# Optimization experiments

Hardware: AMD Instinct MI355X
Metric: run time of the kernel (lower is better)

The kernel has to match this reference:

```python
import jax, jax.numpy as jnp
import numpy as np

_SAMPLING_EPS = 1e-05
_FP16_TINY = float(np.finfo(np.float16).tiny)  # masked_fill value used by the torch code


def _token_mask(tokens, num_seqs, vocab_size):
    # bin-count via scatter-add into width vocab+1 (padding id == vocab), then mask
    rows = jnp.arange(num_seqs)[:, None]
    counts = jnp.zeros((num_seqs, vocab_size + 1), jnp.int32).at[rows, tokens].add(1)
    return counts[:, :vocab_size] > 0


def setup_inputs() -> dict:
    key = jax.random.key(0)
    ks = jax.random.split(key, 9)
    B, V, PL, OL = 128, 128000, 2048, 256
    logits = jax.random.normal(ks[0], (B, V), dtype=jnp.float32) * 4.0
    prompt_tokens = jax.random.randint(ks[1], (B, PL), 0, V, dtype=jnp.int64)
    output_tokens = jax.random.randint(ks[2], (B, OL), 0, V, dtype=jnp.int64)
    presence_penalties = jax.random.uniform(ks[3], (B,), dtype=jnp.float32)
    frequency_penalties = jax.random.uniform(ks[4], (B,), dtype=jnp.float32)
    repetition_penalties = 1.0 + 0.3 * jax.random.uniform(ks[5], (B,), dtype=jnp.float32)
    temperature = 0.1 + 0.9 * jax.random.uniform(ks[6], (B,), dtype=jnp.float32)
    top_k = jax.random.randint(ks[7], (B,), 1, 100, dtype=jnp.int64)
    top_p = 0.5 + 0.49 * jax.random.uniform(ks[8], (B,), dtype=jnp.float32)
    return {
        "logits": logits,
        "prompt_tokens": prompt_tokens,
        "output_tokens": output_tokens,
        "presence_penalties": presence_penalties,
        "frequency_penalties": frequency_penalties,
        "repetition_penalties": repetition_penalties,
        "temperature": temperature,
        "top_k": top_k,
        "top_p": top_p,
    }


def reference(logits, prompt_tokens, output_tokens, presence_penalties,
              frequency_penalties, repetition_penalties, temperature,
              top_k, top_p):
    B, V = logits.shape
    logits = logits.astype(jnp.float32)

    # --- penalties (NOTE: torch code computes frequency counts but never applies
    # frequency_penalties; we faithfully do the same) ---
    prompt_mask = _token_mask(prompt_tokens, B, V)
    output_mask = _token_mask(output_tokens, B, V)
    pen = jnp.where(prompt_mask | output_mask, repetition_penalties[:, None], 1.0)
    logits = jnp.where(logits > 0, logits / pen, logits * pen)
    logits = logits - presence_penalties[:, None] * output_mask.astype(jnp.float32)

    # --- temperature ---
    temp = jnp.where(temperature < _SAMPLING_EPS, 1.0, temperature)
    logits = logits / temp[:, None]

    # --- top-k / top-p via ascending sort (mirrors torch implementation) ---
    idx = jnp.argsort(logits, axis=-1)                      # ascending
    ls = jnp.take_along_axis(logits, idx, axis=-1)
    thr_pos = (V - top_k.astype(jnp.int32))[:, None]
    thr = jnp.take_along_axis(ls, thr_pos, axis=-1)         # [B,1]
    ls = jnp.where(ls < thr, _FP16_TINY, ls)
    probs_sort = jax.nn.softmax(ls, axis=-1)
    csum = jnp.cumsum(probs_sort, axis=-1)
    tp_mask = csum <= (1.0 - top_p)[:, None]
    tp_mask = tp_mask.at[:, -1].set(False)
    ls = jnp.where(tp_mask, _FP16_TINY, ls)

    # unsort back to original vocab order
    rows = jnp.arange(B)[:, None]
    out_logits = jnp.zeros_like(logits).at[rows, idx].set(ls)

    probs = jax.nn.softmax(out_logits, axis=-1)
    return probs, prompt_mask, output_mask
```

## Files before the change

kernel.cpp:

```cpp
#include <hip/hip_runtime.h>
#include <math.h>

#define B   128
#define V   128000
#define WPR 4000
#define PL  2048
#define OL  256
#define BPR 25
#define ITERS 5
#define TLOC 128
#define CAP  6144
#define FP16_TINY 6.103515625e-05f

#define HBINS 4096
#define HIDX(b) ((b) + ((b) >> 4))
#define HSZ (HBINS + (HBINS >> 4))

__device__ __forceinline__ unsigned key_of(float f) {
    unsigned u = __float_as_uint(f);
    unsigned m = (unsigned)(((int)u) >> 31) | 0x80000000u;
    return u ^ m;
}
__device__ __forceinline__ float key_inv(unsigned k) {
    unsigned u = (k & 0x80000000u) ? (k ^ 0x80000000u) : ~k;
    return __uint_as_float(u);
}

__device__ __forceinline__ float xform(float x, int pm, int om,
                                       float rp, float rrp, float pres, float itt) {
#pragma clang fp contract(off)
    float m = (pm | om) ? ((x > 0.0f) ? rrp : rp) : 1.0f;
    float l = x * m;
    if (om) l = l - pres;
    return l * itt;
}

__device__ __forceinline__ unsigned wave_suffix_u(unsigned x, int lane) {
#pragma unroll
    for (int o = 1; o < 64; o <<= 1) {
        unsigned a = __shfl_down(x, o);
        if (lane + o < 64) x += a;
    }
    return x;
}
__device__ __forceinline__ unsigned wave_prefix_u(unsigned x, int lane) {
#pragma unroll
    for (int o = 1; o < 64; o <<= 1) {
        unsigned a = __shfl_up(x, o);
        if (lane >= o) x += a;
    }
    return x;
}
__device__ __forceinline__ double wave_suffix_d(double x, int lane) {
#pragma unroll
    for (int o = 1; o < 64; o <<= 1) {
        double a = __shfl_down(x, o);
        if (lane + o < 64) x += a;
    }
    return x;
}
__device__ __forceinline__ double wave_sum_d(double x) {
#pragma unroll
    for (int o = 1; o < 64; o <<= 1) x += __shfl_xor(x, o);
    return x;
}
__device__ __forceinline__ unsigned wave_sum_u(unsigned x) {
#pragma unroll
    for (int o = 1; o < 64; o <<= 1) x += __shfl_xor(x, o);
    return x;
}

__global__ __launch_bounds__(256) void k_scatter(const int* __restrict__ ptok,
                                                 const int* __restrict__ otok,
                                                 unsigned* __restrict__ bitP,
                                                 unsigned* __restrict__ bitO,
                                                 unsigned* __restrict__ cnt) {
    __shared__ unsigned mp[WPR];
    __shared__ unsigned mo[WPR];
    int r = blockIdx.x;
    int t = threadIdx.x;
    for (int i = t; i < WPR; i += 256) { mp[i] = 0u; mo[i] = 0u; }
    if (t == 0) cnt[r] = 0u;
    __syncthreads();
    const int* prow = ptok + (size_t)r * PL;
    const int* orow = otok + (size_t)r * OL;
    for (int i = t; i < PL; i += 256) {
        int tok = prow[i];
        if ((unsigned)tok < (unsigned)V) atomicOr(&mp[tok >> 5], 1u << (tok & 31));
    }
    for (int i = t; i < OL; i += 256) {
        int tok = orow[i];
        if ((unsigned)tok < (unsigned)V) atomicOr(&mo[tok >> 5], 1u << (tok & 31));
    }
    __syncthreads();
    unsigned* bpo = bitP + (size_t)r * WPR;
    unsigned* boo = bitO + (size_t)r * WPR;
    for (int i = t; i < WPR; i += 256) { bpo[i] = mp[i]; boo[i] = mo[i]; }
}

__global__ __launch_bounds__(256) void k_main(
    const float* __restrict__ logits,
    const unsigned* __restrict__ bitP, const unsigned* __restrict__ bitO,
    const float* __restrict__ rep, const float* __restrict__ pres,
    const float* __restrict__ temp,
    float* __restrict__ outPm, float* __restrict__ outOm,
    unsigned* __restrict__ cnt, unsigned long long* __restrict__ cand)
{
    __shared__ unsigned h[HSZ];
    __shared__ unsigned wsum[4];
    __shared__ int s_beta;
    __shared__ unsigned s_base;
    int r = blockIdx.y;
    int c0 = blockIdx.x * (ITERS * 1024);
    int t = threadIdx.x;
    int lane = t & 63, wid = t >> 6;
    for (int i = t; i < HSZ; i += 256) h[i] = 0u;
    __syncthreads();
    float rp = rep[r], pp = pres[r];
    float tt = temp[r]; tt = (tt < 1e-5f) ? 1.0f : tt;
    float rrp = 1.0f / rp;
    float itt = 1.0f / tt;
    const float* lrow = logits + (size_t)r * V;
    float* pmrow = outPm + (size_t)r * V;
    float* omrow = outOm + (size_t)r * V;
    const unsigned* bp = bitP + (size_t)r * WPR;
    const unsigned* bo = bitO + (size_t)r * WPR;
    uint4 kv4[ITERS];
#pragma unroll
    for (int it = 0; it < ITERS; it++) {
        int i = c0 + it * 1024 + t * 4;
        float4 x = *(const float4*)(lrow + i);
        unsigned wp = bp[i >> 5], wo = bo[i >> 5];
        int sh = i & 31;
        float xs[4] = {x.x, x.y, x.z, x.w};
        unsigned ks[4];
        float fp[4], fo[4];
#pragma unroll
        for (int j = 0; j < 4; j++) {
            int p = (wp >> (sh + j)) & 1;
            int o = (wo >> (sh + j)) & 1;
            float l = xform(xs[j], p, o, rp, rrp, pp, itt);
            unsigned key = key_of(l);
            atomicAdd(&h[HIDX(key >> 20)], 1u);
            ks[j] = key; fp[j] = (float)p; fo[j] = (float)o;
        }
        kv4[it] = make_uint4(ks[0], ks[1], ks[2], ks[3]);
        *(float4*)(pmrow + i) = make_float4(fp[0], fp[1], fp[2], fp[3]);
        *(float4*)(omrow + i) = make_float4(fo[0], fo[1], fo[2], fo[3]);
    }
    __syncthreads();
    unsigned cs = 0;
#pragma unroll
    for (int j = 0; j < 16; j++) cs += h[HIDX(t * 16 + j)];
    unsigned sfx = wave_suffix_u(cs, lane);
    if (lane == 0) wsum[wid] = sfx;
    __syncthreads();
    unsigned suf = sfx;
#pragma unroll
    for (int w2 = 0; w2 < 4; w2++) if (w2 > wid) suf += wsum[w2];
    unsigned Snext = suf - cs;
    if (suf >= TLOC && Snext < TLOC) {
        unsigned run = Snext;
        int beta = t * 16;
        for (int j = 15; j >= 0; j--) {
            run += h[HIDX(t * 16 + j)];
            if (run >= TLOC) { beta = t * 16 + j; break; }
        }
        s_beta = beta;
    }
    __syncthreads();
    unsigned beta = (unsigned)s_beta;
    unsigned myc = 0;
#pragma unroll
    for (int it = 0; it < ITERS; it++) {
        unsigned ks[4] = {kv4[it].x, kv4[it].y, kv4[it].z, kv4[it].w};
#pragma unroll
        for (int j = 0; j < 4; j++)
            if ((ks[j] >> 20) >= beta) myc++;
    }
    unsigned pfx = wave_prefix_u(myc, lane);
    if (lane == 63) wsum[wid] = pfx;
    __syncthreads();
    unsigned pv = pfx;
#pragma unroll
    for (int w2 = 0; w2 < 4; w2++) if (w2 < wid) pv += wsum[w2];
    if (t == 255) s_base = atomicAdd(&cnt[r], pv);
    __syncthreads();
    unsigned w = s_base + (pv - myc);
#pragma unroll
    for (int it = 0; it < ITERS; it++) {
        unsigned ks[4] = {kv4[it].x, kv4[it].y, kv4[it].z, kv4[it].w};
#pragma unroll
        for (int j = 0; j < 4; j++) {
            unsigned key = ks[j];
            if ((key >> 20) >= beta) {
                if (w < (unsigned)CAP) {
                    int idx = c0 + it * 1024 + t * 4 + j;
                    cand[(size_t)r * CAP + w] =
                        ((unsigned long long)key << 32) | (unsigned)idx;
                }
                w++;
            }
        }
    }
}

__global__ __launch_bounds__(256) void k_select(
    const unsigned* __restrict__ cnt, const unsigned long long* __restrict__ cand,
    const int* __restrict__ topk, const float* __restrict__ topp,
    float4* __restrict__ params, int* __restrict__ idxc)
{
    __shared__ unsigned long long list[CAP];
    __shared__ unsigned long long kv[256];
    __shared__ unsigned rh[256];
    __shared__ double wD[4];
    __shared__ unsigned wU[4];
    __shared__ unsigned s_prefix, s_krem, s_kcnt;
    int r = blockIdx.x;
    int t = threadIdx.x;
    int lane = t & 63, wid = t >> 6;
    int n = (int)min(cnt[r], (unsigned)CAP);
    const unsigned long long* crow = cand + (size_t)r * CAP;
    for (int i = t; i < n; i += 256) list[i] = crow[i];
    int k = topk[r]; k = max(1, min(k, 127));
    if (t == 0) { s_prefix = 0u; s_krem = (unsigned)k; }
    __syncthreads();
    for (int round = 3; round >= 0; round--) {
        int shift = round * 8;
        unsigned prefix = s_prefix;
        unsigned krem = s_krem;
        unsigned maskAbove = (round == 3) ? 0u : (0xFFFFFFFFu << (shift + 8));
        rh[t] = 0u;
        __syncthreads();
        for (int i = t; i < n; i += 256) {
            unsigned key = (unsigned)(list[i] >> 32);
            if ((key & maskAbove) == (prefix & maskAbove))
                atomicAdd(&rh[(key >> shift) & 255u], 1u);
        }
        __syncthreads();
        unsigned vv = rh[t];
        unsigned sfx = wave_suffix_u(vv, lane);
        if (lane == 0) wU[wid] = sfx;
        __syncthreads();
        unsigned suf = sfx;
#pragma unroll
        for (int w2 = 0; w2 < 4; w2++) if (w2 > wid) suf += wU[w2];
        unsigned Sx = suf - vv;
        if (suf >= krem && Sx < krem) {
            s_prefix = prefix | ((unsigned)t << shift);
            s_krem = krem - Sx;
        }
        __syncthreads();
    }
    unsigned thrkey = s_prefix;
    if (t == 0) s_kcnt = 0u;
    __syncthreads();
    for (int i = t; i < n; i += 256) {
        if ((unsigned)(list[i] >> 32) >= thrkey) {
            unsigned pos = atomicAdd(&s_kcnt, 1u);
            if (pos < 256u) kv[pos] = list[i];
        }
    }
    __syncthreads();
    int K = (int)min(s_kcnt, 256u);
    if (t >= K) kv[t] = 0ULL;
    __syncthreads();
    for (unsigned k2 = 2; k2 <= 256; k2 <<= 1) {
        for (unsigned j2 = k2 >> 1; j2 > 0; j2 >>= 1) {
            unsigned ixj = (unsigned)t ^ j2;
            if (ixj > (unsigned)t) {
                unsigned long long a = kv[t], b = kv[ixj];
                bool descBlock = (((unsigned)t & k2) == 0u);
                bool doSwap = descBlock ? (a < b) : (a > b);
                if (doSwap) { kv[t] = b; kv[ixj] = a; }
            }
            __syncthreads();
        }
    }
    float Mxf = key_inv((unsigned)(kv[0] >> 32));
    double MxD = (double)Mxf;
    double e_t = (t < K) ? exp((double)key_inv((unsigned)(kv[t] >> 32)) - MxD)
                         : 0.0;
    double red = wave_sum_d(e_t);
    if (lane == 0) wD[wid] = red;
    __syncthreads();
    double S = wD[0] + wD[1] + wD[2] + wD[3];
    __syncthreads();
    double sv = wave_suffix_d(e_t, lane);
    if (lane == 0) wD[wid] = sv;
    __syncthreads();
    double suf_t = sv;
#pragma unroll
    for (int w2 = 0; w2 < 4; w2++) if (w2 > wid) suf_t += wD[w2];
    double e_tinyD = exp((double)FP16_TINY - MxD);
    double Z1 = (double)(V - K) * e_tinyD + S;
    double base = (double)(V - K) * e_tinyD / Z1;
    double thresh = 1.0 - (double)topp[r];
    unsigned flag = (t >= 1 && t < K && (base + suf_t / Z1) <= thresh) ? 1u : 0u;
    unsigned fr = wave_sum_u(flag);
    if (lane == 0) wU[wid] = fr;
    __syncthreads();
    int cm = (int)(wU[0] + wU[1] + wU[2] + wU[3]);
    int ns = K - cm;
    __syncthreads();
    double e2 = (t < ns) ? e_t : 0.0;
    double r2 = wave_sum_d(e2);
    if (lane == 0) wD[wid] = r2;
    __syncthreads();
    if (t == 0) {
        double S2 = wD[0] + wD[1] + wD[2] + wD[3];
        unsigned bkey = (unsigned)(kv[ns - 1] >> 32);
        float v_b = key_inv(bkey);
        unsigned idx_cut = (unsigned)(kv[ns - 1] & 0xFFFFFFFFu);
        float tiny_e = expf(FP16_TINY - Mxf);
        double Z2 = (double)(V - ns) * (double)tiny_e + S2;
        float invZ2 = (float)(1.0 / Z2);
        params[r] = make_float4(v_b, Mxf, invZ2, tiny_e * invZ2);
        idxc[r] = (int)idx_cut;
    }
}

__global__ __launch_bounds__(256) void k_final(
    const float* __restrict__ logits,
    const unsigned* __restrict__ bitP, const unsigned* __restrict__ bitO,
    const float* __restrict__ rep, const float* __restrict__ pres,
    const float* __restrict__ temp,
    const float4* __restrict__ params, const int* __restrict__ idxc,
    float* __restrict__ probs)
{
    int r = blockIdx.y;
    int c0 = blockIdx.x * (ITERS * 1024);
    int t = threadIdx.x;
    float rp = rep[r], pp = pres[r];
    float tt = temp[r]; tt = (tt < 1e-5f) ? 1.0f : tt;
    float rrp = 1.0f / rp;
    float itt = 1.0f / tt;
    float4 pr = params[r];
    float v_b = pr.x, Mx = pr.y, invZ2 = pr.z, ptiny = pr.w;
    unsigned idx_cut = (unsigned)idxc[r];
    const float* lrow = logits + (size_t)r * V;
    float* orow = probs + (size_t)r * V;
    const unsigned* bp = bitP + (size_t)r * WPR;
    const unsigned* bo = bitO + (size_t)r * WPR;
#pragma unroll
    for (int it = 0; it < ITERS; it++) {
        int i = c0 + it * 1024 + t * 4;
        float4 x = *(const float4*)(lrow + i);
        unsigned wp = bp[i >> 5], wo = bo[i >> 5];
        int sh = i & 31;
        float xs[4] = {x.x, x.y, x.z, x.w};
        float res[4];
#pragma unroll
        for (int j = 0; j < 4; j++) {
            int p = (wp >> (sh + j)) & 1;
            int o = (wo >> (sh + j)) & 1;
            float l = xform(xs[j], p, o, rp, rrp, pp, itt);
            bool keep = (l > v_b) || (l == v_b && (unsigned)(i + j) >= idx_cut);
            res[j] = keep ? (expf(l - Mx) * invZ2) : ptiny;
        }
        *(float4*)(orow + i) = make_float4(res[0], res[1], res[2], res[3]);
    }
}

extern "C" void kernel_launch(void* const* d_in, const int* in_sizes, int n_in,
                              void* d_out, int out_size, void* d_ws, size_t ws_size,
                              hipStream_t stream) {
    const float* logits = (const float*)d_in[0];
    const int* ptok     = (const int*)d_in[1];
    const int* otok     = (const int*)d_in[2];
    const float* pres   = (const float*)d_in[3];
    const float* rep    = (const float*)d_in[5];
    const float* temp   = (const float*)d_in[6];
    const int* topk     = (const int*)d_in[7];
    const float* topp   = (const float*)d_in[8];

    float* out_probs = (float*)d_out;
    float* out_pm = out_probs + (size_t)B * V;
    float* out_om = out_pm + (size_t)B * V;

    unsigned* ws0 = (unsigned*)d_ws;
    float4* params = (float4*)d_ws;
    int* idxc = (int*)(ws0 + 512);
    unsigned* bitP = ws0 + 768;
    unsigned* bitO = bitP + B * WPR;
    unsigned* cnt  = bitO + B * WPR;
    unsigned long long* cand =
        (unsigned long long*)(cnt + B + 64);

    k_scatter<<<B, 256, 0, stream>>>(ptok, otok, bitP, bitO, cnt);

    dim3 g(BPR, B);
    k_main<<<g, 256, 0, stream>>>(logits, bitP, bitO, rep, pres, temp,
                                  out_pm, out_om, cnt, cand);
    k_select<<<B, 256, 0, stream>>>(cnt, cand, topk, topp, params, idxc);
    k_final<<<g, 256, 0, stream>>>(logits, bitP, bitO, rep, pres, temp,
                                   params, idxc, out_probs);
}
```

Measured before the change: 304.2 us.

## Fuse scatter, main, select and final stages into one cooperative kernel

Replaces the four-kernel pipeline with a single cooperative-groups kernel over a fixed grid of 640 blocks. Grid-wide syncs separate the stages: zeroing the bitmaps, scattering tokens with global atomicOr spread across the whole grid, building the histogram and candidate list, per-row top-k/top-p selection, and the final softmax write. The aim is to remove kernel-launch gaps and to parallelize the token scatter beyond one block per row. In exchange it adds grid-sync cost, leaves most blocks idle during the select phase (only 128 of 640 work), and uses global atomics for the scatter. If the cooperative launch fails, it falls back to the old four-kernel path.

```diff
diff --git a/kernel.cpp b/kernel.cpp
--- a/kernel.cpp
+++ b/kernel.cpp
@@ -1,5 +1,8 @@
 #include <hip/hip_runtime.h>
+#include <hip/hip_cooperative_groups.h>
 #include <math.h>
+
+namespace cg = cooperative_groups;
 
 #define B   128
 #define V   128000
@@ -7,6 +10,9 @@
 #define PL  2048
 #define OL  256
 #define BPR 25
+#define NVB 3200
+#define GRID 640
+#define VB_ITERS 5
 #define ITERS 5
 #define TLOC 128
 #define CAP  6144
@@ -68,6 +74,294 @@
 #pragma unroll
     for (int o = 1; o < 64; o <<= 1) x += __shfl_xor(x, o);
     return x;
+}
+
+__global__ __launch_bounds__(256, 4) void k_fused(
+    const float* __restrict__ logits,
+    const int* __restrict__ ptok, const int* __restrict__ otok,
+    const float* __restrict__ rep, const float* __restrict__ pres,
+    const float* __restrict__ temp,
+    const int* __restrict__ topk, const float* __restrict__ topp,
+    float* __restrict__ outPm, float* __restrict__ outOm,
+    float* __restrict__ probs,
+    unsigned* __restrict__ bitP, unsigned* __restrict__ bitO,
+    unsigned* __restrict__ cnt, unsigned long long* __restrict__ cand,
+    float4* __restrict__ params, int* __restrict__ idxc)
+{
+    cg::grid_group gg = cg::this_grid();
+    __shared__ alignas(16) unsigned smem[HSZ];
+    __shared__ unsigned wsum[4];
+    __shared__ double wD[4];
+    __shared__ unsigned wU[4];
+    __shared__ int s_beta;
+    __shared__ unsigned s_base, s_prefix, s_krem, s_kcnt;
+
+    int bid = blockIdx.x;
+    int t = threadIdx.x;
+    int lane = t & 63, wid = t >> 6;
+
+    {
+        int n = 2 * B * WPR + B;
+        for (int i = bid * 256 + t; i < n; i += GRID * 256) bitP[i] = 0u;
+    }
+    gg.sync();
+
+    {
+        int np = B * PL;
+        int total = np + B * OL;
+        for (int i = bid * 256 + t; i < total; i += GRID * 256) {
+            if (i < np) {
+                int r = i >> 11;
+                int tok = ptok[i];
+                if ((unsigned)tok < (unsigned)V)
+                    atomicOr(&bitP[r * WPR + (tok >> 5)], 1u << (tok & 31));
+            } else {
+                int j = i - np;
+                int r = j >> 8;
+                int tok = otok[j];
+                if ((unsigned)tok < (unsigned)V)
+                    atomicOr(&bitO[r * WPR + (tok >> 5)], 1u << (tok & 31));
+            }
+        }
+    }
+    gg.sync();
+
+    for (int kk = 0; kk < VB_ITERS; kk++) {
+        int vb = bid + kk * GRID;
+        int r = vb & 127;
+        int c0 = (vb >> 7) * (ITERS * 1024);
+        for (int i = t; i < HSZ; i += 256) smem[i] = 0u;
+        __syncthreads();
+        float rp = rep[r], pp = pres[r];
+        float tt = temp[r]; tt = (tt < 1e-5f) ? 1.0f : tt;
+        float rrp = 1.0f / rp;
+        float itt = 1.0f / tt;
+        const float* lrow = logits + (size_t)r * V;
+        float* pmrow = outPm + (size_t)r * V;
+        float* omrow = outOm + (size_t)r * V;
+        const unsigned* bp = bitP + (size_t)r * WPR;
+        const unsigned* bo = bitO + (size_t)r * WPR;
+        uint4 kv4[ITERS];
+#pragma unroll
+        for (int it = 0; it < ITERS; it++) {
+            int i = c0 + it * 1024 + t * 4;
+            float4 x = *(const float4*)(lrow + i);
+            unsigned wp = bp[i >> 5], wo = bo[i >> 5];
+            int sh = i & 31;
+            float xs[4] = {x.x, x.y, x.z, x.w};
+            unsigned ks[4];
+            float fp[4], fo[4];
+#pragma unroll
+            for (int j = 0; j < 4; j++) {
+                int p = (wp >> (sh + j)) & 1;
+                int o = (wo >> (sh + j)) & 1;
+                float l = xform(xs[j], p, o, rp, rrp, pp, itt);
+                unsigned key = key_of(l);
+                atomicAdd(&smem[HIDX(key >> 20)], 1u);
+                ks[j] = key; fp[j] = (float)p; fo[j] = (float)o;
+            }
+            kv4[it] = make_uint4(ks[0], ks[1], ks[2], ks[3]);
+            *(float4*)(pmrow + i) = make_float4(fp[0], fp[1], fp[2], fp[3]);
+            *(float4*)(omrow + i) = make_float4(fo[0], fo[1], fo[2], fo[3]);
+        }
+        __syncthreads();
+        unsigned cs = 0;
+#pragma unroll
+        for (int j = 0; j < 16; j++) cs += smem[HIDX(t * 16 + j)];
+        unsigned sfx = wave_suffix_u(cs, lane);
+        if (lane == 0) wsum[wid] = sfx;
+        __syncthreads();
+        unsigned suf = sfx;
+#pragma unroll
+        for (int w2 = 0; w2 < 4; w2++) if (w2 > wid) suf += wsum[w2];
+        unsigned Snext = suf - cs;
+        if (suf >= TLOC && Snext < TLOC) {
+            unsigned run = Snext;
+            int beta = t * 16;
+            for (int j = 15; j >= 0; j--) {
+                run += smem[HIDX(t * 16 + j)];
+                if (run >= TLOC) { beta = t * 16 + j; break; }
+            }
+            s_beta = beta;
+        }
+        __syncthreads();
+        unsigned beta = (unsigned)s_beta;
+        unsigned myc = 0;
+#pragma unroll
+        for (int it = 0; it < ITERS; it++) {
+            unsigned ks[4] = {kv4[it].x, kv4[it].y, kv4[it].z, kv4[it].w};
+#pragma unroll
+            for (int j = 0; j < 4; j++)
+                if ((ks[j] >> 20) >= beta) myc++;
+        }
+        unsigned pfx = wave_prefix_u(myc, lane);
+        if (lane == 63) wsum[wid] = pfx;
+        __syncthreads();
+        unsigned pv = pfx;
+#pragma unroll
+        for (int w2 = 0; w2 < 4; w2++) if (w2 < wid) pv += wsum[w2];
+        if (t == 255) s_base = atomicAdd(&cnt[r], pv);
+        __syncthreads();
+        unsigned w = s_base + (pv - myc);
+#pragma unroll
+        for (int it = 0; it < ITERS; it++) {
+            unsigned ks[4] = {kv4[it].x, kv4[it].y, kv4[it].z, kv4[it].w};
+#pragma unroll
+            for (int j = 0; j < 4; j++) {
+                unsigned key = ks[j];
+                if ((key >> 20) >= beta) {
+                    if (w < (unsigned)CAP) {
+                        int idx = c0 + it * 1024 + t * 4 + j;
+                        cand[(size_t)r * CAP + w] =
+                            ((unsigned long long)key << 32) | (unsigned)idx;
+                    }
+                    w++;
+                }
+            }
+        }
+        __syncthreads();
+    }
+    gg.sync();
+
+    if (bid < B) {
+        int r = bid;
+        unsigned long long* kv = (unsigned long long*)smem;
+        unsigned* rh = smem + 512;
+        int n = (int)min(cnt[r], (unsigned)CAP);
+        const unsigned long long* crow = cand + (size_t)r * CAP;
+        int k = topk[r]; k = max(1, min(k, 127));
+        if (t == 0) { s_prefix = 0u; s_krem = (unsigned)k; }
+        __syncthreads();
+        for (int round = 3; round >= 0; round--) {
+            int shift = round * 8;
+            unsigned prefix = s_prefix;
+            unsigned krem = s_krem;
+            unsigned maskAbove = (round == 3) ? 0u : (0xFFFFFFFFu << (shift + 8));
+            rh[t] = 0u;
+            __syncthreads();
+            for (int i = t; i < n; i += 256) {
+                unsigned key = (unsigned)(crow[i] >> 32);
+                if ((key & maskAbove) == (prefix & maskAbove))
+                    atomicAdd(&rh[(key >> shift) & 255u], 1u);
+            }
+            __syncthreads();
+            unsigned vv = rh[t];
+            unsigned sfx = wave_suffix_u(vv, lane);
+            if (lane == 0) wU[wid] = sfx;
+            __syncthreads();
+            unsigned suf = sfx;
+#pragma unroll
+            for (int w2 = 0; w2 < 4; w2++) if (w2 > wid) suf += wU[w2];
+            unsigned Sx = suf - vv;
+            if (suf >= krem && Sx < krem) {
+                s_prefix = prefix | ((unsigned)t << shift);
+                s_krem = krem - Sx;
+            }
+            __syncthreads();
+        }
+        unsigned thrkey = s_prefix;
+        if (t == 0) s_kcnt = 0u;
+        __syncthreads();
+        for (int i = t; i < n; i += 256) {
+            if ((unsigned)(crow[i] >> 32) >= thrkey) {
+                unsigned pos = atomicAdd(&s_kcnt, 1u);
+                if (pos < 256u) kv[pos] = crow[i];
+            }
+        }
+        __syncthreads();
+        int K = (int)min(s_kcnt, 256u);
+        if (t >= K) kv[t] = 0ULL;
+        __syncthreads();
+        for (unsigned k2 = 2; k2 <= 256; k2 <<= 1) {
+            for (unsigned j2 = k2 >> 1; j2 > 0; j2 >>= 1) {
+                unsigned ixj = (unsigned)t ^ j2;
+                if (ixj > (unsigned)t) {
+                    unsigned long long a = kv[t], b = kv[ixj];
+                    bool descBlock = (((unsigned)t & k2) == 0u);
+                    bool doSwap = descBlock ? (a < b) : (a > b);
+                    if (doSwap) { kv[t] = b; kv[ixj] = a; }
+                }
+                __syncthreads();
+            }
+        }
+        float Mxf = key_inv((unsigned)(kv[0] >> 32));
+        double MxD = (double)Mxf;
+        double e_t = (t < K) ? exp((double)key_inv((unsigned)(kv[t] >> 32)) - MxD)
+                             : 0.0;
+        double red = wave_sum_d(e_t);
+        if (lane == 0) wD[wid] = red;
+        __syncthreads();
+        double S = wD[0] + wD[1] + wD[2] + wD[3];
+        __syncthreads();
+        double sv = wave_suffix_d(e_t, lane);
+        if (lane == 0) wD[wid] = sv;
+        __syncthreads();
+        double suf_t = sv;
+#pragma unroll
+        for (int w2 = 0; w2 < 4; w2++) if (w2 > wid) suf_t += wD[w2];
+        double e_tinyD = exp((double)FP16_TINY - MxD);
+        double Z1 = (double)(V - K) * e_tinyD + S;
+        double base = (double)(V - K) * e_tinyD / Z1;
+        double thresh = 1.0 - (double)topp[r];
+        unsigned flag = (t >= 1 && t < K && (base + suf_t / Z1) <= thresh) ? 1u : 0u;
+        unsigned fr = wave_sum_u(flag);
+        if (lane == 0) wU[wid] = fr;
+        __syncthreads();
+        int cm = (int)(wU[0] + wU[1] + wU[2] + wU[3]);
+        int ns = K - cm;
+        __syncthreads();
+        double e2 = (t < ns) ? e_t : 0.0;
+        double r2 = wave_sum_d(e2);
+        if (lane == 0) wD[wid] = r2;
+        __syncthreads();
+        if (t == 0) {
+            double S2 = wD[0] + wD[1] + wD[2] + wD[3];
+            unsigned bkey = (unsigned)(kv[ns - 1] >> 32);
+            float v_b = key_inv(bkey);
+            unsigned idx_cut = (unsigned)(kv[ns - 1] & 0xFFFFFFFFu);
+            float tiny_e = expf(FP16_TINY - Mxf);
+            double Z2 = (double)(V - ns) * (double)tiny_e + S2;
+            float invZ2 = (float)(1.0 / Z2);
+            params[r] = make_float4(v_b, Mxf, invZ2, tiny_e * invZ2);
+            idxc[r] = (int)idx_cut;
+        }
+    }
+    gg.sync();
+
+    for (int kk = 0; kk < VB_ITERS; kk++) {
+        int vb = bid + kk * GRID;
+        int r = vb & 127;
+        int c0 = (vb >> 7) * (ITERS * 1024);
+        float rp = rep[r], pp = pres[r];
+        float tt = temp[r]; tt = (tt < 1e-5f) ? 1.0f : tt;
+        float rrp = 1.0f / rp;
+        float itt = 1.0f / tt;
+        float4 pr = params[r];
+        float v_b = pr.x, Mx = pr.y, invZ2 = pr.z, ptiny = pr.w;
+        unsigned idx_cut = (unsigned)idxc[r];
+        const float* lrow = logits + (size_t)r * V;
+        float* orow = probs + (size_t)r * V;
+        const unsigned* bp = bitP + (size_t)r * WPR;
+        const unsigned* bo = bitO + (size_t)r * WPR;
+#pragma unroll
+        for (int it = 0; it < ITERS; it++) {
+            int i = c0 + it * 1024 + t * 4;
+            float4 x = *(const float4*)(lrow + i);
+            unsigned wp = bp[i >> 5], wo = bo[i >> 5];
+            int sh = i & 31;
+            float xs[4] = {x.x, x.y, x.z, x.w};
+            float res[4];
+#pragma unroll
+            for (int j = 0; j < 4; j++) {
+                int p = (wp >> (sh + j)) & 1;
+                int o = (wo >> (sh + j)) & 1;
+                float l = xform(xs[j], p, o, rp, rrp, pp, itt);
+                bool keep = (l > v_b) || (l == v_b && (unsigned)(i + j) >= idx_cut);
+                res[j] = keep ? (expf(l - Mx) * invZ2) : ptiny;
+            }
+            *(float4*)(orow + i) = make_float4(res[0], res[1], res[2], res[3]);
+        }
+    }
 }
 
 __global__ __launch_bounds__(256) void k_scatter(const int* __restrict__ ptok,
@@ -387,12 +681,24 @@
     unsigned long long* cand =
         (unsigned long long*)(cnt + B + 64);
 
-    k_scatter<<<B, 256, 0, stream>>>(ptok, otok, bitP, bitO, cnt);
-
-    dim3 g(BPR, B);
-    k_main<<<g, 256, 0, stream>>>(logits, bitP, bitO, rep, pres, temp,
-                                  out_pm, out_om, cnt, cand);
-    k_select<<<B, 256, 0, stream>>>(cnt, cand, topk, topp, params, idxc);
-    k_final<<<g, 256, 0, stream>>>(logits, bitP, bitO, rep, pres, temp,
-                                   params, idxc, out_probs);
-}
+    void* args[] = {
+        (void*)&logits, (void*)&ptok, (void*)&otok,
+        (void*)&rep, (void*)&pres, (void*)&temp,
+        (void*)&topk, (void*)&topp,
+        (void*)&out_pm, (void*)&out_om, (void*)&out_probs,
+        (void*)&bitP, (void*)&bitO, (void*)&cnt, (void*)&cand,
+        (void*)&params, (void*)&idxc,
+    };
+    hipError_t err = hipLaunchCooperativeKernel((void*)k_fused, dim3(GRID),
+                                                dim3(256), args, 0, stream);
+    if (err != hipSuccess) {
+        (void)hipGetLastError();
+        k_scatter<<<B, 256, 0, stream>>>(ptok, otok, bitP, bitO, cnt);
+        dim3 g(BPR, B);
+        k_main<<<g, 256, 0, stream>>>(logits, bitP, bitO, rep, pres, temp,
+                                      out_pm, out_om, cnt, cand);
+        k_select<<<B, 256, 0, stream>>>(cnt, cand, topk, topp, params, idxc);
+        k_final<<<g, 256, 0, stream>>>(logits, bitP, bitO, rep, pres, temp,
+                                       params, idxc, out_probs);
+    }
+}
```

Result: slower. 588.5 us (+93.4%).

## Write kept top-k probabilities as sparse list; final pass fills tiny constant

Applied to the files above, without the earlier changes.

k_select now emits, for each row, the indices of the surviving top-k/top-p tokens and their final probabilities. k_final no longer re-reads logits or penalty bitmasks or recomputes exp. It fills the output with the constant tiny probability and then scatters the few kept entries within its column range. This removes a full logits read and per-element arithmetic from the last pass, at the cost of a block barrier and a short per-block scan over the kept list.

```diff
diff --git a/kernel.cpp b/kernel.cpp
--- a/kernel.cpp
+++ b/kernel.cpp
@@ -208,7 +208,8 @@
 __global__ __launch_bounds__(256) void k_select(
     const unsigned* __restrict__ cnt, const unsigned long long* __restrict__ cand,
     const int* __restrict__ topk, const float* __restrict__ topp,
-    float4* __restrict__ params, int* __restrict__ idxc)
+    float4* __restrict__ params, int* __restrict__ idxc,
+    unsigned* __restrict__ kn, int* __restrict__ kidx, float* __restrict__ kprob)
 {
     __shared__ unsigned long long list[CAP];
     __shared__ unsigned long long kv[256];
@@ -307,58 +308,47 @@
     double r2 = wave_sum_d(e2);
     if (lane == 0) wD[wid] = r2;
     __syncthreads();
+    double S2 = wD[0] + wD[1] + wD[2] + wD[3];
+    unsigned bkey = (unsigned)(kv[ns - 1] >> 32);
+    float v_b = key_inv(bkey);
+    float tiny_e = expf(FP16_TINY - Mxf);
+    double Z2 = (double)(V - ns) * (double)tiny_e + S2;
+    float invZ2 = (float)(1.0 / Z2);
     if (t == 0) {
-        double S2 = wD[0] + wD[1] + wD[2] + wD[3];
-        unsigned bkey = (unsigned)(kv[ns - 1] >> 32);
-        float v_b = key_inv(bkey);
-        unsigned idx_cut = (unsigned)(kv[ns - 1] & 0xFFFFFFFFu);
-        float tiny_e = expf(FP16_TINY - Mxf);
-        double Z2 = (double)(V - ns) * (double)tiny_e + S2;
-        float invZ2 = (float)(1.0 / Z2);
         params[r] = make_float4(v_b, Mxf, invZ2, tiny_e * invZ2);
-        idxc[r] = (int)idx_cut;
+        idxc[r] = (int)(kv[ns - 1] & 0xFFFFFFFFu);
+        kn[r] = (unsigned)ns;
+    }
+    if (t < ns) {
+        unsigned long long e = kv[t];
+        unsigned key = (unsigned)(e >> 32);
+        kidx[(size_t)r * 256 + t] = (int)(e & 0xFFFFFFFFu);
+        kprob[(size_t)r * 256 + t] = expf(key_inv(key) - Mxf) * invZ2;
     }
 }
 
 __global__ __launch_bounds__(256) void k_final(
-    const float* __restrict__ logits,
-    const unsigned* __restrict__ bitP, const unsigned* __restrict__ bitO,
-    const float* __restrict__ rep, const float* __restrict__ pres,
-    const float* __restrict__ temp,
-    const float4* __restrict__ params, const int* __restrict__ idxc,
+    const float4* __restrict__ params, const unsigned* __restrict__ kn,
+    const int* __restrict__ kidx, const float* __restrict__ kprob,
     float* __restrict__ probs)
 {
     int r = blockIdx.y;
     int c0 = blockIdx.x * (ITERS * 1024);
     int t = threadIdx.x;
-    float rp = rep[r], pp = pres[r];
-    float tt = temp[r]; tt = (tt < 1e-5f) ? 1.0f : tt;
-    float rrp = 1.0f / rp;
-    float itt = 1.0f / tt;
-    float4 pr = params[r];
-    float v_b = pr.x, Mx = pr.y, invZ2 = pr.z, ptiny = pr.w;
-    unsigned idx_cut = (unsigned)idxc[r];
-    const float* lrow = logits + (size_t)r * V;
+    float ptiny = params[r].w;
     float* orow = probs + (size_t)r * V;
-    const unsigned* bp = bitP + (size_t)r * WPR;
-    const unsigned* bo = bitO + (size_t)r * WPR;
+    float4 pv4 = make_float4(ptiny, ptiny, ptiny, ptiny);
 #pragma unroll
     for (int it = 0; it < ITERS; it++) {
         int i = c0 + it * 1024 + t * 4;
-        float4 x = *(const float4*)(lrow + i);
-        unsigned wp = bp[i >> 5], wo = bo[i >> 5];
-        int sh = i & 31;
-        float xs[4] = {x.x, x.y, x.z, x.w};
-        float res[4];
-#pragma unroll
-        for (int j = 0; j < 4; j++) {
-            int p = (wp >> (sh + j)) & 1;
-            int o = (wo >> (sh + j)) & 1;
-            float l = xform(xs[j], p, o, rp, rrp, pp, itt);
-            bool keep = (l > v_b) || (l == v_b && (unsigned)(i + j) >= idx_cut);
-            res[j] = keep ? (expf(l - Mx) * invZ2) : ptiny;
-        }
-        *(float4*)(orow + i) = make_float4(res[0], res[1], res[2], res[3]);
+        *(float4*)(orow + i) = pv4;
+    }
+    __syncthreads();
+    int ns = (int)kn[r];
+    int hi = c0 + ITERS * 1024;
+    for (int i = t; i < ns; i += 256) {
+        int idx = kidx[(size_t)r * 256 + i];
+        if (idx >= c0 && idx < hi) orow[idx] = kprob[(size_t)r * 256 + i];
     }
 }
 
@@ -386,13 +376,16 @@
     unsigned* cnt  = bitO + B * WPR;
     unsigned long long* cand =
         (unsigned long long*)(cnt + B + 64);
+    unsigned* kn   = (unsigned*)(cand + (size_t)B * CAP);
+    int* kidx      = (int*)(kn + B);
+    float* kprob   = (float*)(kidx + B * 256);
 
     k_scatter<<<B, 256, 0, stream>>>(ptok, otok, bitP, bitO, cnt);
 
     dim3 g(BPR, B);
     k_main<<<g, 256, 0, stream>>>(logits, bitP, bitO, rep, pres, temp,
                                   out_pm, out_om, cnt, cand);
-    k_select<<<B, 256, 0, stream>>>(cnt, cand, topk, topp, params, idxc);
-    k_final<<<g, 256, 0, stream>>>(logits, bitP, bitO, rep, pres, temp,
-                                   params, idxc, out_probs);
-}
+    k_select<<<B, 256, 0, stream>>>(cnt, cand, topk, topp, params, idxc,
+                                    kn, kidx, kprob);
+    k_final<<<g, 256, 0, stream>>>(params, kn, kidx, kprob, out_probs);
+}
```

Result: faster. 297.5 us (-2.2%).
